# Optimization experiments

Measured on AMD Instinct MI355X. Metric: run time of the kernel, lower is better.

## Reference

```python
import jax, jax.numpy as jnp
import numpy as np

EXP_SCALE = 10.0   # self.exp_param_scale
BETA_UP = 5.0      # self.kernel_beta_upbound
N_HEAD = 12


def setup_inputs() -> dict:
    key = jax.random.key(0)
    ks = jax.random.split(key, 7)
    B, T, C, nh = 2, 2048, 768, N_HEAD
    s = 1.0 / np.sqrt(C)
    x = jax.random.normal(ks[0], (B, T, C), jnp.float32)
    W_la = jax.random.normal(ks[1], (C, C), jnp.float32) * s      # LeakyAverage linear
    la_coef = jax.random.uniform(ks[2], (nh,), jnp.float32)        # per-head leaky decay in (0,1)
    W_v = jax.random.normal(ks[3], (C, C), jnp.float32) * s        # v_featurizer linear
    v_coef = jax.random.uniform(ks[4], (nh,), jnp.float32)         # v_featurizer per-head coef
    kernel_beta = jnp.ones((nh,), jnp.float32) / EXP_SCALE
    value_beta = jnp.ones((nh,), jnp.float32) * (-0.5 / EXP_SCALE)
    W_proj = jax.random.normal(ks[5], (C, C), jnp.float32) * s     # c_proj
    return dict(x=x, W_la=W_la, la_coef=la_coef, W_v=W_v, v_coef=v_coef,
                kernel_beta=kernel_beta, value_beta=value_beta, W_proj=W_proj)


def _leaky_average(x, W_la, la_coef):
    # y_t = c * y_{t-1} + (1-c) * (x W^T)_t, per-head decay c. Returns (B, nh, T, hs).
    B, T, C = x.shape
    nh = la_coef.shape[0]
    hs = C // nh
    u = (x @ W_la.T).reshape(B, T, nh, hs)
    c = la_coef[None, :, None]  # (1, nh, 1) broadcast over (B, nh, hs)

    def step(carry, ut):
        y = c * carry + (1.0 - c) * ut
        return y, y

    _, ys = jax.lax.scan(step, jnp.zeros((B, nh, hs), x.dtype), jnp.swapaxes(u, 0, 1))
    return jnp.transpose(ys, (1, 2, 0, 3))  # (T,B,nh,hs) -> (B,nh,T,hs)


def reference(x, W_la, la_coef, W_v, v_coef, kernel_beta, value_beta, W_proj):
    B, T, C = x.shape
    nh = la_coef.shape[0]
    hs = C // nh
    v_shift = 1

    # K path: leaky-average features, L2-normalize, exp-kernel beta scale
    k0 = _leaky_average(x, W_la, la_coef)                               # (B,nh,T,hs)
    raw_k = k0 / (jnp.linalg.norm(k0, axis=-1, keepdims=True) + 1e-6)
    beta = jnp.exp(jnp.minimum(kernel_beta * EXP_SCALE, BETA_UP))
    k = raw_k * beta[None, :, None, None]

    # V path: lowrlinearconv featurizer (linear, shift-by-1 mix, normalize) + value scale
    xl = (x @ W_v.T).reshape(B, T, nh, hs).transpose(0, 2, 1, 3)        # (B,nh,T,hs)
    shifted = jnp.concatenate([xl[:, :, 1:], jnp.zeros_like(xl[:, :, :1])], axis=2)
    vc = v_coef[None, :, None, None]
    vf = shifted * (1.0 - vc) + xl * vc
    vf = vf / (jnp.linalg.norm(vf, axis=-1, keepdims=True) + 1e-6)
    vbeta = jnp.exp(jnp.minimum(value_beta * EXP_SCALE, BETA_UP))
    v = vf * vbeta[None, :, None, None]

    # shifted-causal attention: query at position t (t>=1) attends keys 0..t-1, scale=1.0
    q = k[:, :, v_shift:]                                               # (B,nh,T-1,hs)
    scores = jnp.einsum('bhqd,bhkd->bhqk', q, k)                        # (B,nh,T-1,T)
    mask = jnp.tril(jnp.ones((T - v_shift, T), bool))                   # j <= iq  <=>  key < query pos
    scores = jnp.where(mask, scores, -jnp.inf)
    attn = jax.nn.softmax(scores, axis=-1)
    o = jnp.einsum('bhqk,bhkd->bhqd', attn, v)
    y = jnp.concatenate([jnp.zeros((B, nh, v_shift, hs), x.dtype), o], axis=2)

    y = y.transpose(0, 2, 1, 3).reshape(B, T, C)
    return y @ W_proj.T  # c_proj (dropouts are identity in eval)
```

## Files before the change

### kernel.cpp

```cpp
#include <hip/hip_runtime.h>
#include <hip/hip_bf16.h>
#include <math.h>

#define B_   2
#define T_   2048
#define C_   768
#define NH   12
#define HS   64
#define NSEG 64
#define SEGLEN 32
#define CX   1536

typedef __attribute__((ext_vector_type(8))) short short8;
typedef __attribute__((ext_vector_type(4))) short short4v;
typedef __attribute__((ext_vector_type(4))) float f32x4;
typedef __attribute__((ext_vector_type(16))) float f32x16;
typedef __attribute__((ext_vector_type(2))) unsigned int uint2v;
typedef __attribute__((ext_vector_type(4))) unsigned int uint4v;

static __device__ inline unsigned short f2b(float f) {
  __hip_bfloat16 h = __float2bfloat16(f);
  unsigned short u;
  __builtin_memcpy(&u, &h, 2);
  return u;
}
static __device__ inline float b2f(unsigned short u) {
  unsigned int x = ((unsigned int)u) << 16;
  float f;
  __builtin_memcpy(&f, &x, 4);
  return f;
}
static __device__ inline unsigned cvtpk(float a, float b) {
  unsigned r;
  asm("v_cvt_pk_bf16_f32 %0, %1, %2" : "=v"(r) : "v"(a), "v"(b));
  return r;
}

#define GLOAD_LDS16(gp, lp)                                                        \
  __builtin_amdgcn_global_load_lds((const __attribute__((address_space(1))) void*)(gp), \
                                   (__attribute__((address_space(3))) void*)(lp), 16, 0, 0)

__global__ __launch_bounds__(256) void cast_all(const float* __restrict__ x,
                                                const float* __restrict__ wla,
                                                const float* __restrict__ wv,
                                                const float* __restrict__ wp,
                                                __hip_bfloat16* __restrict__ xb,
                                                __hip_bfloat16* __restrict__ wcat,
                                                __hip_bfloat16* __restrict__ wpb) {
  const int NX4 = (B_ * T_ * C_) / 4;
  const int NW4 = (C_ * C_) / 4;
  const int TOT = NX4 + 3 * NW4;
  int i = blockIdx.x * 256 + threadIdx.x;
  int st = gridDim.x * 256;
  for (; i < TOT; i += st) {
    const float* s;
    unsigned short* d;
    if (i < NX4) { s = x + (size_t)i * 4; d = (unsigned short*)xb + (size_t)i * 4; }
    else if (i < NX4 + NW4) { int j = i - NX4; s = wla + (size_t)j * 4; d = (unsigned short*)wcat + (size_t)j * 4; }
    else if (i < NX4 + 2 * NW4) { int j = i - NX4 - NW4; s = wv + (size_t)j * 4; d = (unsigned short*)wcat + (size_t)(C_ * C_) + (size_t)j * 4; }
    else { int j = i - NX4 - 2 * NW4; s = wp + (size_t)j * 4; d = (unsigned short*)wpb + (size_t)j * 4; }
    float4 v = *(const float4*)s;
    short4v o;
    o.x = (short)f2b(v.x); o.y = (short)f2b(v.y); o.z = (short)f2b(v.z); o.w = (short)f2b(v.w);
    *(short4v*)d = o;
  }
}

template <int BM, bool OB16>
__global__ __launch_bounds__(256) void gemm_bf16(const __hip_bfloat16* __restrict__ A,
                                                 const __hip_bfloat16* __restrict__ Bw,
                                                 void* __restrict__ Cv,
                                                 int M, int N, int K) {
  __shared__ __hip_bfloat16 As[BM * 64];
  __shared__ __hip_bfloat16 Bs[128 * 64];
  const int tid = threadIdx.x;
  const int w = tid >> 6, lane = tid & 63;
  const int bm = blockIdx.x * BM, bn = blockIdx.y * 128;
  const int q16 = lane & 15, lg = lane >> 4;

  constexpr int NACC = (BM == 128) ? 4 : 2;
  f32x4 acc[4][NACC];
#pragma unroll
  for (int i = 0; i < 4; ++i)
#pragma unroll
    for (int j = 0; j < NACC; ++j) acc[i][j] = (f32x4){0.f, 0.f, 0.f, 0.f};

  const int srow = (lane >> 3);
  const int soff0 = (lane & 7) * 16;
  const int sw = (lane & 7) << 4;
  constexpr int ACH = BM / 8;
  constexpr int CPW = (ACH + 16) / 4;

  for (int k0 = 0; k0 < K; k0 += 64) {
    __syncthreads();
#pragma unroll
    for (int c = 0; c < CPW; ++c) {
      int gc = w * CPW + c;
      int isB = gc >= ACH;
      int ci = isB ? gc - ACH : gc;
      int row = ci * 8 + srow;
      int soff = soff0 ^ ((row & 7) << 4);
      const __hip_bfloat16* gp =
          (isB ? Bw + (size_t)(bn + row) * K : A + (size_t)(bm + row) * K) + k0 + (soff >> 1);
      __hip_bfloat16* lp = (isB ? Bs : As) + ci * 512;
      GLOAD_LDS16(gp, lp);
    }
    __syncthreads();
#pragma unroll
    for (int ks = 0; ks < 2; ++ks) {
      short8 af[4], bf[NACC];
      const int colb = ks * 64 + lg * 16;
#pragma unroll
      for (int i = 0; i < 4; ++i) {
        int ra = (BM == 128) ? ((w >> 1) * 64 + i * 16 + q16) : (i * 16 + q16);
        af[i] = *(const short8*)((const char*)As + ra * 128 + (colb ^ sw));
      }
#pragma unroll
      for (int j = 0; j < NACC; ++j) {
        int rb = (BM == 128) ? ((w & 1) * 64 + j * 16 + q16) : (w * 32 + j * 16 + q16);
        bf[j] = *(const short8*)((const char*)Bs + rb * 128 + (colb ^ sw));
      }
#pragma unroll
      for (int i = 0; i < 4; ++i)
#pragma unroll
        for (int j = 0; j < NACC; ++j)
          acc[i][j] = __builtin_amdgcn_mfma_f32_16x16x32_bf16(af[i], bf[j], acc[i][j], 0, 0, 0);
    }
  }
#pragma unroll
  for (int i = 0; i < 4; ++i) {
#pragma unroll
    for (int r = 0; r < 4; ++r) {
      int m = (BM == 128) ? (bm + (w >> 1) * 64 + i * 16 + lg * 4 + r)
                          : (bm + i * 16 + lg * 4 + r);
      int nb = (BM == 128) ? (bn + (w & 1) * 64 + q16) : (bn + w * 32 + q16);
      if (OB16) {
        unsigned short* cp = (unsigned short*)Cv + (size_t)m * N + nb;
#pragma unroll
        for (int j = 0; j < NACC; ++j) cp[j * 16] = f2b(acc[i][j][r]);
      } else {
        float* cp = (float*)Cv + (size_t)m * N + nb;
#pragma unroll
        for (int j = 0; j < NACC; ++j) cp[j * 16] = acc[i][j][r];
      }
    }
  }
}

__global__ __launch_bounds__(256) void scan_seg(const unsigned short* __restrict__ uxv,
                                                const float* __restrict__ la_coef,
                                                float* __restrict__ segend) {
  int cid = blockIdx.x * 4 + (threadIdx.x >> 6);
  int d   = threadIdx.x & 63;
  int seg = cid & (NSEG - 1);
  int bh  = cid >> 6;
  int h   = bh % NH;
  int b   = bh / NH;
  float c  = la_coef[h];
  float oc = 1.f - c;
  int t0 = seg * SEGLEN;
  const unsigned short* up = uxv + ((size_t)b * T_ + t0) * CX + h * HS + d;
  float uv[SEGLEN];
#pragma unroll
  for (int i = 0; i < SEGLEN; ++i) uv[i] = b2f(up[(size_t)i * CX]);
  float y = 0.f;
#pragma unroll
  for (int i = 0; i < SEGLEN; ++i) y = fmaf(c, y, oc * uv[i]);
  segend[(size_t)cid * HS + d] = y;
}

__global__ __launch_bounds__(256) void scan_b(const float* __restrict__ la_coef,
                                              const float* __restrict__ segend,
                                              float* __restrict__ carryin) {
  int s = blockIdx.x * 256 + threadIdx.x;
  if (s >= B_ * NH * HS) return;
  int d  = s & 63;
  int bh = s >> 6;
  int h  = bh % NH;
  float c = la_coef[h];
  float cl = c;
#pragma unroll
  for (int i = 0; i < 5; ++i) cl *= cl;
  float h0 = 0.f;
  for (int seg = 0; seg < NSEG; ++seg) {
    int cid = bh * NSEG + seg;
    carryin[(size_t)cid * HS + d] = h0;
    h0 = fmaf(cl, h0, segend[(size_t)cid * HS + d]);
  }
}

__global__ __launch_bounds__(256) void scanc_vbuild(const float* __restrict__ la_coef,
                                                    const float* __restrict__ kernel_beta,
                                                    const float* __restrict__ carryin,
                                                    const unsigned short* __restrict__ uxv,
                                                    const float* __restrict__ v_coef,
                                                    const float* __restrict__ value_beta,
                                                    __hip_bfloat16* __restrict__ kb16,
                                                    __hip_bfloat16* __restrict__ vt) {
  __shared__ __hip_bfloat16 sm[64][73];
  const int NBC = B_ * NH * NSEG / 4;
  if ((int)blockIdx.x < NBC) {
    int cid = blockIdx.x * 4 + (threadIdx.x >> 6);
    int d   = threadIdx.x & 63;
    int seg = cid & (NSEG - 1);
    int bh  = cid >> 6;
    int h   = bh % NH;
    int b   = bh / NH;
    float c  = la_coef[h];
    float oc = 1.f - c;
    float bk = __expf(fminf(kernel_beta[h] * 10.f, 5.f));
    int t0 = seg * SEGLEN;
    const unsigned short* up = uxv + ((size_t)b * T_ + t0) * CX + h * HS + d;
    __hip_bfloat16* op = kb16 + ((size_t)bh * T_ + t0) * HS + d;
    float uv[SEGLEN];
#pragma unroll
    for (int i = 0; i < SEGLEN; ++i) uv[i] = b2f(up[(size_t)i * CX]);
    float y = carryin[(size_t)cid * HS + d];
    for (int i = 0; i < SEGLEN; ++i) {
      y = fmaf(c, y, oc * uv[i]);
      float ss = y * y;
#pragma unroll
      for (int off = 1; off < 64; off <<= 1) ss += __shfl_xor(ss, off, 64);
      float scale = bk / (sqrtf(ss) + 1e-6f);
      op[(size_t)i * HS] = __float2bfloat16(y * scale);
    }
  } else {
    int idx = blockIdx.x - NBC;
    int t0 = (idx & 31) * 64;
    int bh = idx >> 5;
    int h = bh % NH, b = bh / NH;
    int w = threadIdx.x >> 6, lane = threadIdx.x & 63;
    float vc = v_coef[h];
    float vb = __expf(fminf(value_beta[h] * 10.f, 5.f));
    for (int i = 0; i < 16; ++i) {
      int tl = w * 16 + i;
      int t = t0 + tl;
      const unsigned short* xp = uxv + ((size_t)b * T_ + t) * CX + 768 + h * HS + lane;
      float x0 = b2f(*xp);
      float x1 = (t + 1 < T_) ? b2f(xp[CX]) : 0.f;
      float vf = (1.f - vc) * x1 + vc * x0;
      float ss = vf * vf;
#pragma unroll
      for (int off = 1; off < 64; off <<= 1) ss += __shfl_xor(ss, off, 64);
      sm[tl][lane] = __float2bfloat16(vf * vb / (sqrtf(ss) + 1e-6f));
    }
    __syncthreads();
    int d = threadIdx.x >> 3;
    int c = threadIdx.x & 7;
    for (int i = 0; i < 2; ++i) {
      int dd = d + i * 32;
      short8 v;
#pragma unroll
      for (int k = 0; k < 8; ++k)
        v[k] = (short)((const unsigned short*)&sm[c * 8 + k][dd])[0];
      *(short8*)((unsigned short*)vt + ((size_t)bh * HS + dd) * T_ + t0 + c * 8) = v;
    }
  }
}

__global__ __launch_bounds__(256, 2) void attn10(const __hip_bfloat16* __restrict__ Kg,
                                                 const __hip_bfloat16* __restrict__ Vtg,
                                                 const float* __restrict__ kernel_beta,
                                                 __hip_bfloat16* __restrict__ Y) {
  __shared__ __align__(16) char lds[33792];
  const int bh = blockIdx.x;
  const int b = bh / NH, h = bh % NH;
  const int w = threadIdx.x >> 6, lane = threadIdx.x & 63;
  const int l31 = lane & 31, lg2 = lane >> 5;
  const int it = 31 - blockIdx.y;
  const int qb0 = 1 + it * 64;
  const int NT32 = 2 * it + 2;
  float bk = __expf(fminf(kernel_beta[h] * 10.f, 5.f));
  const float L2E = 1.4426950408889634f;
  const float m0l = bk * bk * L2E;
  const unsigned short* Kh = (const unsigned short*)Kg + (size_t)bh * T_ * HS;
  const unsigned short* Vh = (const unsigned short*)Vtg + (size_t)bh * HS * T_;
  unsigned short* Yh = (unsigned short*)Y + (size_t)b * T_ * C_ + h * HS;

  if (it == 0 && w == 0) Yh[lane] = 0;

  short8 qf[2][4];
#pragma unroll
  for (int qs = 0; qs < 2; ++qs) {
    int tqc = qb0 + qs * 32 + l31;
    if (tqc > T_ - 1) tqc = T_ - 1;
#pragma unroll
    for (int s = 0; s < 4; ++s)
      qf[qs][s] = *(const short8*)(Kh + (size_t)tqc * HS + s * 16 + lg2 * 8);
  }

  f32x16 zero16 = {0.f};
  f32x16 accO[2][2];
#pragma unroll
  for (int qs = 0; qs < 2; ++qs)
#pragma unroll
    for (int ds = 0; ds < 2; ++ds) accO[qs][ds] = zero16;
  float lsum[2] = {0.f, 0.f};

#define LOADT(KF, VF, j0)                                                             \
  {                                                                                   \
    _Pragma("unroll")                                                                 \
    for (int s = 0; s < 4; ++s)                                                       \
      KF[s] = *(const short8*)(Kh + (size_t)((j0) + l31) * HS + s * 16 + lg2 * 8);    \
    _Pragma("unroll")                                                                 \
    for (int ds = 0; ds < 2; ++ds)                                                    \
      _Pragma("unroll")                                                               \
      for (int s2 = 0; s2 < 2; ++s2)                                                  \
        VF[ds][s2] = *(const short8*)(Vh + (size_t)(ds * 32 + l31) * T_ + (j0) +      \
                                      s2 * 16 + lg2 * 8);                             \
  }

#define COMPUTE(KF, VF, ktv)                                                          \
  {                                                                                   \
    const int j0c = (ktv)*32;                                                         \
    const int jb = j0c + 4 * lg2;                                                     \
    _Pragma("unroll")                                                                 \
    for (int qs = 0; qs < 2; ++qs) {                                                  \
      const int tqq = qb0 + qs * 32 + l31;                                            \
      f32x16 S = zero16;                                                              \
      __builtin_amdgcn_s_setprio(1);                                                  \
      _Pragma("unroll")                                                               \
      for (int s = 0; s < 4; ++s)                                                     \
        S = __builtin_amdgcn_mfma_f32_32x32x16_bf16(KF[s], qf[qs][s], S, 0, 0, 0);    \
      __builtin_amdgcn_s_setprio(0);                                                  \
      float p[16];                                                                    \
      _Pragma("unroll")                                                               \
      for (int r = 0; r < 16; ++r) {                                                  \
        int jg = jb + (r & 3) + 8 * (r >> 2);                                         \
        p[r] = (jg < tqq) ? exp2f(fmaf(S[r], L2E, -m0l)) : 0.f;                       \
        lsum[qs] += p[r];                                                             \
      }                                                                               \
      uint2v g00 = __builtin_amdgcn_permlane32_swap(cvtpk(p[0], p[1]),                \
                                                    cvtpk(p[4], p[5]), false, false); \
      uint2v g01 = __builtin_amdgcn_permlane32_swap(cvtpk(p[2], p[3]),                \
                                                    cvtpk(p[6], p[7]), false, false); \
      uint2v g10 = __builtin_amdgcn_permlane32_swap(cvtpk(p[8], p[9]),                \
                                                    cvtpk(p[12], p[13]), false, false);\
      uint2v g11 = __builtin_amdgcn_permlane32_swap(cvtpk(p[10], p[11]),              \
                                                    cvtpk(p[14], p[15]), false, false);\
      uint4v pb0v, pb1v;                                                              \
      pb0v.x = g00.x; pb0v.y = g01.x; pb0v.z = g00.y; pb0v.w = g01.y;                 \
      pb1v.x = g10.x; pb1v.y = g11.x; pb1v.z = g10.y; pb1v.w = g11.y;                 \
      short8 PB0 = __builtin_bit_cast(short8, pb0v);                                  \
      short8 PB1 = __builtin_bit_cast(short8, pb1v);                                  \
      __builtin_amdgcn_s_setprio(1);                                                  \
      _Pragma("unroll")                                                               \
      for (int ds = 0; ds < 2; ++ds) {                                                \
        accO[qs][ds] = __builtin_amdgcn_mfma_f32_32x32x16_bf16(VF[ds][0], PB0,        \
                                                               accO[qs][ds], 0, 0, 0);\
        accO[qs][ds] = __builtin_amdgcn_mfma_f32_32x32x16_bf16(VF[ds][1], PB1,        \
                                                               accO[qs][ds], 0, 0, 0);\
      }                                                                               \
      __builtin_amdgcn_s_setprio(0);                                                  \
    }                                                                                 \
  }

  short8 kfA[4], vfA[2][2], kfB[4], vfB[2][2];
  int kt = w;
  if (kt < NT32) LOADT(kfA, vfA, kt * 32);
  while (kt < NT32) {
    if (kt + 4 < NT32) LOADT(kfB, vfB, (kt + 4) * 32);
    COMPUTE(kfA, vfA, kt);
    kt += 4;
    if (kt >= NT32) break;
    if (kt + 4 < NT32) LOADT(kfA, vfA, (kt + 4) * 32);
    COMPUTE(kfB, vfB, kt);
    kt += 4;
  }

#pragma unroll
  for (int qs = 0; qs < 2; ++qs) lsum[qs] += __shfl_xor(lsum[qs], 32, 64);

  float* LR = (float*)(lds + 32768);
  __syncthreads();
  if (w >= 2) {
    float* PB = (float*)(lds + (size_t)(w - 2) * 16384);
#pragma unroll
    for (int qs = 0; qs < 2; ++qs)
#pragma unroll
      for (int ds = 0; ds < 2; ++ds)
        *(f32x16*)(PB + ((qs * 2 + ds) * 64 + lane) * 16) = accO[qs][ds];
  }
#pragma unroll
  for (int qs = 0; qs < 2; ++qs) LR[(w * 2 + qs) * 32 + l31] = lsum[qs];
  __syncthreads();
  if (w < 2) {
    float* PB = (float*)(lds + (size_t)w * 16384);
#pragma unroll
    for (int qs = 0; qs < 2; ++qs)
#pragma unroll
      for (int ds = 0; ds < 2; ++ds) {
        f32x16 o = *(f32x16*)(PB + ((qs * 2 + ds) * 64 + lane) * 16);
#pragma unroll
        for (int r = 0; r < 16; ++r) accO[qs][ds][r] += o[r];
      }
    if (w == 1) {
#pragma unroll
      for (int qs = 0; qs < 2; ++qs)
#pragma unroll
        for (int ds = 0; ds < 2; ++ds)
          *(f32x16*)(PB + ((qs * 2 + ds) * 64 + lane) * 16) = accO[qs][ds];
    }
  }
  __syncthreads();
  if (w == 0) {
    float* PB1 = (float*)(lds + 16384);
#pragma unroll
    for (int qs = 0; qs < 2; ++qs) {
#pragma unroll
      for (int ds = 0; ds < 2; ++ds) {
        f32x16 o = *(f32x16*)(PB1 + ((qs * 2 + ds) * 64 + lane) * 16);
#pragma unroll
        for (int r = 0; r < 16; ++r) accO[qs][ds][r] += o[r];
      }
      float tot = LR[(0 * 2 + qs) * 32 + l31] + LR[(1 * 2 + qs) * 32 + l31] +
                  LR[(2 * 2 + qs) * 32 + l31] + LR[(3 * 2 + qs) * 32 + l31];
      float inv = 1.f / tot;
      int tq = qb0 + qs * 32 + l31;
      if (tq < T_) {
        unsigned short* yp = Yh + (size_t)tq * C_;
#pragma unroll
        for (int ds = 0; ds < 2; ++ds)
#pragma unroll
          for (int r = 0; r < 16; r += 2) {
            int d = ds * 32 + (r & 3) + 8 * (r >> 2) + 4 * lg2;
            unsigned u = cvtpk(accO[qs][ds][r] * inv, accO[qs][ds][r + 1] * inv);
            *(unsigned*)(yp + d) = u;
          }
      }
    }
  }
#undef LOADT
#undef COMPUTE
}

extern "C" void kernel_launch(void* const* d_in, const int* in_sizes, int n_in,
                              void* d_out, int out_size, void* d_ws, size_t ws_size,
                              hipStream_t stream) {
  const float* x          = (const float*)d_in[0];
  const float* W_la       = (const float*)d_in[1];
  const float* la_coef    = (const float*)d_in[2];
  const float* W_v        = (const float*)d_in[3];
  const float* v_coef     = (const float*)d_in[4];
  const float* kernel_bet = (const float*)d_in[5];
  const float* value_bet  = (const float*)d_in[6];
  const float* W_proj     = (const float*)d_in[7];
  float* out = (float*)d_out;

  char* ws = (char*)d_ws;
  const size_t NTOK = (size_t)B_ * T_ * C_;
  const size_t NSEGTOT = (size_t)B_ * NH * NSEG * HS;
  unsigned short* uxv = (unsigned short*)ws;
  float* segend  = (float*)(ws + (size_t)B_ * T_ * CX * 2);
  float* carryin = segend + NSEGTOT;
  __hip_bfloat16* kb16 = (__hip_bfloat16*)(carryin + NSEGTOT);
  __hip_bfloat16* vt16 = kb16 + NTOK;
  __hip_bfloat16* xb   = vt16 + NTOK;
  __hip_bfloat16* Wcat = xb + NTOK;
  __hip_bfloat16* Wpb  = Wcat + (size_t)CX * C_;
  __hip_bfloat16* yb   = xb;

  const int M = B_ * T_;

  cast_all<<<2048, 256, 0, stream>>>(x, W_la, W_v, W_proj, xb, Wcat, Wpb);

  gemm_bf16<64, true><<<dim3(M / 64, CX / 128), 256, 0, stream>>>(xb, Wcat, uxv, M, CX, C_);

  scan_seg<<<dim3(B_ * NH * NSEG / 4), 256, 0, stream>>>(uxv, la_coef, segend);
  scan_b<<<dim3((B_ * NH * HS + 255) / 256), 256, 0, stream>>>(la_coef, segend, carryin);
  scanc_vbuild<<<dim3(B_ * NH * NSEG / 4 + 32 * B_ * NH), 256, 0, stream>>>(
      la_coef, kernel_bet, carryin, uxv, v_coef, value_bet, kb16, vt16);

  attn10<<<dim3(B_ * NH, 32), 256, 0, stream>>>(kb16, vt16, kernel_bet, yb);

  gemm_bf16<64, false><<<dim3(M / 64, C_ / 128), 256, 0, stream>>>(yb, Wpb, out, M, C_, C_);
}
```

Baseline: 101.1 us.

## Split attention into unmasked and masked tile paths, pad LDS reduction, enlarge GEMM tile

The attention kernel now handles fully-below-diagonal key tiles in a loop with no causal mask compare, and runs only the last two diagonal tiles through the masked path without double buffering. The cross-wave LDS reduction buffer uses a padded 20-float row stride with 4-wide stores and loads to reduce bank conflicts, which grows LDS use. Separately, the first QKV GEMM goes from a 64-row to a 128-row M tile. There is an odd comma-expression double store in the reduction, and the masked path drops the setprio hints around the QK MFMAs.

```diff
diff --git a/kernel.cpp b/kernel.cpp
--- a/kernel.cpp
+++ b/kernel.cpp
@@ -258,11 +258,11 @@
   }
 }
 
-__global__ __launch_bounds__(256, 2) void attn10(const __hip_bfloat16* __restrict__ Kg,
+__global__ __launch_bounds__(256, 2) void attn11(const __hip_bfloat16* __restrict__ Kg,
                                                  const __hip_bfloat16* __restrict__ Vtg,
                                                  const float* __restrict__ kernel_beta,
                                                  __hip_bfloat16* __restrict__ Y) {
-  __shared__ __align__(16) char lds[33792];
+  __shared__ __align__(16) char lds[41984];
   const int bh = blockIdx.x;
   const int b = bh / NH, h = bh % NH;
   const int w = threadIdx.x >> 6, lane = threadIdx.x & 63;
@@ -270,6 +270,7 @@
   const int it = 31 - blockIdx.y;
   const int qb0 = 1 + it * 64;
   const int NT32 = 2 * it + 2;
+  const int NTU = NT32 - 2;
   float bk = __expf(fminf(kernel_beta[h] * 10.f, 5.f));
   const float L2E = 1.4426950408889634f;
   const float m0l = bk * bk * L2E;
@@ -310,13 +311,38 @@
                                       s2 * 16 + lg2 * 8);                             \
   }
 
-#define COMPUTE(KF, VF, ktv)                                                          \
+#define PV_STEP(VF, qs)                                                               \
   {                                                                                   \
-    const int j0c = (ktv)*32;                                                         \
-    const int jb = j0c + 4 * lg2;                                                     \
+    __builtin_amdgcn_s_setprio(1);                                                    \
+    _Pragma("unroll")                                                                 \
+    for (int ds = 0; ds < 2; ++ds) {                                                  \
+      accO[qs][ds] = __builtin_amdgcn_mfma_f32_32x32x16_bf16(VF[ds][0], PB0,          \
+                                                             accO[qs][ds], 0, 0, 0);  \
+      accO[qs][ds] = __builtin_amdgcn_mfma_f32_32x32x16_bf16(VF[ds][1], PB1,          \
+                                                             accO[qs][ds], 0, 0, 0);  \
+    }                                                                                 \
+    __builtin_amdgcn_s_setprio(0);                                                    \
+  }
+
+#define PACK_P()                                                                      \
+  uint2v g00 = __builtin_amdgcn_permlane32_swap(cvtpk(p[0], p[1]),                    \
+                                                cvtpk(p[4], p[5]), false, false);     \
+  uint2v g01 = __builtin_amdgcn_permlane32_swap(cvtpk(p[2], p[3]),                    \
+                                                cvtpk(p[6], p[7]), false, false);     \
+  uint2v g10 = __builtin_amdgcn_permlane32_swap(cvtpk(p[8], p[9]),                    \
+                                                cvtpk(p[12], p[13]), false, false);   \
+  uint2v g11 = __builtin_amdgcn_permlane32_swap(cvtpk(p[10], p[11]),                  \
+                                                cvtpk(p[14], p[15]), false, false);   \
+  uint4v pb0v, pb1v;                                                                  \
+  pb0v.x = g00.x; pb0v.y = g01.x; pb0v.z = g00.y; pb0v.w = g01.y;                     \
+  pb1v.x = g10.x; pb1v.y = g11.x; pb1v.z = g10.y; pb1v.w = g11.y;                     \
+  short8 PB0 = __builtin_bit_cast(short8, pb0v);                                      \
+  short8 PB1 = __builtin_bit_cast(short8, pb1v);
+
+#define COMPUTE_U(KF, VF)                                                             \
+  {                                                                                   \
     _Pragma("unroll")                                                                 \
     for (int qs = 0; qs < 2; ++qs) {                                                  \
-      const int tqq = qb0 + qs * 32 + l31;                                            \
       f32x16 S = zero16;                                                              \
       __builtin_amdgcn_s_setprio(1);                                                  \
       _Pragma("unroll")                                                               \
@@ -326,92 +352,120 @@
       float p[16];                                                                    \
       _Pragma("unroll")                                                               \
       for (int r = 0; r < 16; ++r) {                                                  \
+        p[r] = exp2f(fmaf(S[r], L2E, -m0l));                                          \
+        lsum[qs] += p[r];                                                             \
+      }                                                                               \
+      PACK_P();                                                                       \
+      PV_STEP(VF, qs);                                                                \
+    }                                                                                 \
+  }
+
+#define COMPUTE_M(KF, VF, ktv)                                                        \
+  {                                                                                   \
+    const int jb = (ktv)*32 + 4 * lg2;                                                \
+    _Pragma("unroll")                                                                 \
+    for (int qs = 0; qs < 2; ++qs) {                                                  \
+      const int tqq = qb0 + qs * 32 + l31;                                            \
+      f32x16 S = zero16;                                                              \
+      _Pragma("unroll")                                                               \
+      for (int s = 0; s < 4; ++s)                                                     \
+        S = __builtin_amdgcn_mfma_f32_32x32x16_bf16(KF[s], qf[qs][s], S, 0, 0, 0);    \
+      float p[16];                                                                    \
+      _Pragma("unroll")                                                               \
+      for (int r = 0; r < 16; ++r) {                                                  \
         int jg = jb + (r & 3) + 8 * (r >> 2);                                         \
         p[r] = (jg < tqq) ? exp2f(fmaf(S[r], L2E, -m0l)) : 0.f;                       \
         lsum[qs] += p[r];                                                             \
       }                                                                               \
-      uint2v g00 = __builtin_amdgcn_permlane32_swap(cvtpk(p[0], p[1]),                \
-                                                    cvtpk(p[4], p[5]), false, false); \
-      uint2v g01 = __builtin_amdgcn_permlane32_swap(cvtpk(p[2], p[3]),                \
-                                                    cvtpk(p[6], p[7]), false, false); \
-      uint2v g10 = __builtin_amdgcn_permlane32_swap(cvtpk(p[8], p[9]),                \
-                                                    cvtpk(p[12], p[13]), false, false);\
-      uint2v g11 = __builtin_amdgcn_permlane32_swap(cvtpk(p[10], p[11]),              \
-                                                    cvtpk(p[14], p[15]), false, false);\
-      uint4v pb0v, pb1v;                                                              \
-      pb0v.x = g00.x; pb0v.y = g01.x; pb0v.z = g00.y; pb0v.w = g01.y;                 \
-      pb1v.x = g10.x; pb1v.y = g11.x; pb1v.z = g10.y; pb1v.w = g11.y;                 \
-      short8 PB0 = __builtin_bit_cast(short8, pb0v);                                  \
-      short8 PB1 = __builtin_bit_cast(short8, pb1v);                                  \
-      __builtin_amdgcn_s_setprio(1);                                                  \
-      _Pragma("unroll")                                                               \
-      for (int ds = 0; ds < 2; ++ds) {                                                \
-        accO[qs][ds] = __builtin_amdgcn_mfma_f32_32x32x16_bf16(VF[ds][0], PB0,        \
-                                                               accO[qs][ds], 0, 0, 0);\
-        accO[qs][ds] = __builtin_amdgcn_mfma_f32_32x32x16_bf16(VF[ds][1], PB1,        \
-                                                               accO[qs][ds], 0, 0, 0);\
-      }                                                                               \
-      __builtin_amdgcn_s_setprio(0);                                                  \
+      PACK_P();                                                                       \
+      PV_STEP(VF, qs);                                                                \
     }                                                                                 \
   }
 
   short8 kfA[4], vfA[2][2], kfB[4], vfB[2][2];
   int kt = w;
-  if (kt < NT32) LOADT(kfA, vfA, kt * 32);
-  while (kt < NT32) {
-    if (kt + 4 < NT32) LOADT(kfB, vfB, (kt + 4) * 32);
-    COMPUTE(kfA, vfA, kt);
-    kt += 4;
-    if (kt >= NT32) break;
-    if (kt + 4 < NT32) LOADT(kfA, vfA, (kt + 4) * 32);
-    COMPUTE(kfB, vfB, kt);
-    kt += 4;
+  if (kt < NTU) {
+    LOADT(kfA, vfA, kt * 32);
+    while (true) {
+      if (kt + 4 < NTU) LOADT(kfB, vfB, (kt + 4) * 32);
+      COMPUTE_U(kfA, vfA);
+      kt += 4;
+      if (kt >= NTU) break;
+      if (kt + 4 < NTU) LOADT(kfA, vfA, (kt + 4) * 32);
+      COMPUTE_U(kfB, vfB);
+      kt += 4;
+      if (kt >= NTU) break;
+    }
+  }
+  for (; kt < NT32; kt += 4) {
+    LOADT(kfA, vfA, kt * 32);
+    COMPUTE_M(kfA, vfA, kt);
   }
 
 #pragma unroll
   for (int qs = 0; qs < 2; ++qs) lsum[qs] += __shfl_xor(lsum[qs], 32, 64);
 
-  float* LR = (float*)(lds + 32768);
+  float* LR = (float*)(lds + 40960);
   __syncthreads();
   if (w >= 2) {
-    float* PB = (float*)(lds + (size_t)(w - 2) * 16384);
+    float* PB = (float*)(lds + (size_t)(w - 2) * 20480);
 #pragma unroll
     for (int qs = 0; qs < 2; ++qs)
 #pragma unroll
-      for (int ds = 0; ds < 2; ++ds)
-        *(f32x16*)(PB + ((qs * 2 + ds) * 64 + lane) * 16) = accO[qs][ds];
+      for (int ds = 0; ds < 2; ++ds) {
+        float* rb = PB + ((qs * 2 + ds) * 64 + lane) * 20;
+#pragma unroll
+        for (int c = 0; c < 4; ++c)
+          *(f32x4*)(rb + c * 4) = __builtin_shufflevector(
+              accO[qs][ds], accO[qs][ds], 0, 1, 2, 3) ,
+          *(f32x4*)(rb + c * 4) = (f32x4){accO[qs][ds][c * 4 + 0], accO[qs][ds][c * 4 + 1],
+                                          accO[qs][ds][c * 4 + 2], accO[qs][ds][c * 4 + 3]};
+      }
   }
 #pragma unroll
   for (int qs = 0; qs < 2; ++qs) LR[(w * 2 + qs) * 32 + l31] = lsum[qs];
   __syncthreads();
   if (w < 2) {
-    float* PB = (float*)(lds + (size_t)w * 16384);
+    float* PB = (float*)(lds + (size_t)w * 20480);
 #pragma unroll
     for (int qs = 0; qs < 2; ++qs)
 #pragma unroll
       for (int ds = 0; ds < 2; ++ds) {
-        f32x16 o = *(f32x16*)(PB + ((qs * 2 + ds) * 64 + lane) * 16);
-#pragma unroll
-        for (int r = 0; r < 16; ++r) accO[qs][ds][r] += o[r];
+        float* rb = PB + ((qs * 2 + ds) * 64 + lane) * 20;
+#pragma unroll
+        for (int c = 0; c < 4; ++c) {
+          f32x4 o = *(f32x4*)(rb + c * 4);
+          accO[qs][ds][c * 4 + 0] += o[0]; accO[qs][ds][c * 4 + 1] += o[1];
+          accO[qs][ds][c * 4 + 2] += o[2]; accO[qs][ds][c * 4 + 3] += o[3];
+        }
       }
     if (w == 1) {
 #pragma unroll
       for (int qs = 0; qs < 2; ++qs)
 #pragma unroll
-        for (int ds = 0; ds < 2; ++ds)
-          *(f32x16*)(PB + ((qs * 2 + ds) * 64 + lane) * 16) = accO[qs][ds];
+        for (int ds = 0; ds < 2; ++ds) {
+          float* rb = PB + ((qs * 2 + ds) * 64 + lane) * 20;
+#pragma unroll
+          for (int c = 0; c < 4; ++c)
+            *(f32x4*)(rb + c * 4) = (f32x4){accO[qs][ds][c * 4 + 0], accO[qs][ds][c * 4 + 1],
+                                            accO[qs][ds][c * 4 + 2], accO[qs][ds][c * 4 + 3]};
+        }
     }
   }
   __syncthreads();
   if (w == 0) {
-    float* PB1 = (float*)(lds + 16384);
+    float* PB1 = (float*)(lds + 20480);
 #pragma unroll
     for (int qs = 0; qs < 2; ++qs) {
 #pragma unroll
       for (int ds = 0; ds < 2; ++ds) {
-        f32x16 o = *(f32x16*)(PB1 + ((qs * 2 + ds) * 64 + lane) * 16);
-#pragma unroll
-        for (int r = 0; r < 16; ++r) accO[qs][ds][r] += o[r];
+        float* rb = PB1 + ((qs * 2 + ds) * 64 + lane) * 20;
+#pragma unroll
+        for (int c = 0; c < 4; ++c) {
+          f32x4 o = *(f32x4*)(rb + c * 4);
+          accO[qs][ds][c * 4 + 0] += o[0]; accO[qs][ds][c * 4 + 1] += o[1];
+          accO[qs][ds][c * 4 + 2] += o[2]; accO[qs][ds][c * 4 + 3] += o[3];
+        }
       }
       float tot = LR[(0 * 2 + qs) * 32 + l31] + LR[(1 * 2 + qs) * 32 + l31] +
                   LR[(2 * 2 + qs) * 32 + l31] + LR[(3 * 2 + qs) * 32 + l31];
@@ -431,7 +485,10 @@
     }
   }
 #undef LOADT
-#undef COMPUTE
+#undef COMPUTE_U
+#undef COMPUTE_M
+#undef PACK_P
+#undef PV_STEP
 }
 
 extern "C" void kernel_launch(void* const* d_in, const int* in_sizes, int n_in,
@@ -464,14 +521,14 @@
 
   cast_all<<<2048, 256, 0, stream>>>(x, W_la, W_v, W_proj, xb, Wcat, Wpb);
 
-  gemm_bf16<64, true><<<dim3(M / 64, CX / 128), 256, 0, stream>>>(xb, Wcat, uxv, M, CX, C_);
+  gemm_bf16<128, true><<<dim3(M / 128, CX / 128), 256, 0, stream>>>(xb, Wcat, uxv, M, CX, C_);
 
   scan_seg<<<dim3(B_ * NH * NSEG / 4), 256, 0, stream>>>(uxv, la_coef, segend);
   scan_b<<<dim3((B_ * NH * HS + 255) / 256), 256, 0, stream>>>(la_coef, segend, carryin);
   scanc_vbuild<<<dim3(B_ * NH * NSEG / 4 + 32 * B_ * NH), 256, 0, stream>>>(
       la_coef, kernel_bet, carryin, uxv, v_coef, value_bet, kb16, vt16);
 
-  attn10<<<dim3(B_ * NH, 32), 256, 0, stream>>>(kb16, vt16, kernel_bet, yb);
+  attn11<<<dim3(B_ * NH, 32), 256, 0, stream>>>(kb16, vt16, kernel_bet, yb);
 
   gemm_bf16<64, false><<<dim3(M / 64, C_ / 128), 256, 0, stream>>>(yb, Wpb, out, M, C_, C_);
 }
```

After: 103.8 us. +2.6%, slower.
